# Kernel optimization log

Hardware: AMD Instinct MI355X
Metric: run time of the kernel (lower is better)

The kernel has to match this reference:

```python
import jax, jax.numpy as jnp
import numpy as np

N_IN = 20000
N_OUT = 20000
E = 640000
B = 64


def setup_inputs() -> dict:
    key = jax.random.key(0)
    ks = jax.random.split(key, 6)
    x = jax.random.normal(ks[0], (B, N_IN), dtype=jnp.float32)
    alpha = jax.random.normal(ks[1], (1, N_IN), dtype=jnp.float32) * 0.01  # xavier-ish scale
    sigma = jax.random.uniform(ks[2], (N_IN,), dtype=jnp.float32, minval=0.5, maxval=1.5)
    inp_positions = jax.random.normal(ks[3], (N_IN, 3), dtype=jnp.float32)
    out_positions = jax.random.normal(ks[4], (N_OUT, 3), dtype=jnp.float32)
    dst = jax.random.randint(ks[5], (E,), 0, N_OUT, dtype=jnp.int64)
    src = jax.random.randint(jax.random.fold_in(ks[5], 1), (E,), 0, N_IN, dtype=jnp.int64)
    edge_index = jnp.stack([dst, src], axis=0)  # [2, E]: row0 -> out node, row1 -> in node
    return {"x": x, "alpha": alpha, "sigma": sigma,
            "inp_positions": inp_positions, "out_positions": out_positions,
            "edge_index": edge_index}


def reference(x, alpha, sigma, inp_positions, out_positions, edge_index):
    dst = edge_index[0]  # [E] indexes out_positions
    src = edge_index[1]  # [E] indexes inp_positions
    # Gaussian RBF edge weights: exp(-||p_in - p_out||^2 / sigma_src^2)
    d = inp_positions[src] - out_positions[dst]          # [E, 3]
    w = jnp.exp(-jnp.sum(d * d, axis=-1) / (sigma[src] ** 2))  # [E]
    # spmm: y[b, i] = sum_{e: dst=i} w_e * (alpha * x)[b, src_e]
    msg = (alpha * x)[:, src] * w                         # [B, E]
    y = jax.ops.segment_sum(msg.T, dst, num_segments=out_positions.shape[0])  # [N_out, B]
    return y.T                                            # [B, N_out]
```

## Files before the change

kernel.cpp:

```cpp
#include <hip/hip_runtime.h>
#include <hip/hip_fp16.h>

#define N_IN   20000
#define N_OUT  20000
#define NEDGE  640000
#define B      64
#define NB     1250
#define CAPB   32
#define BTOT   768
#define CHUNK  8192
#define PBLK   79

__global__ __launch_bounds__(256)
void prep_partition_kernel(const int* __restrict__ edge,
                           unsigned int* __restrict__ gbuf,
                           int* __restrict__ cnt2d,
                           const float* __restrict__ x,
                           const float* __restrict__ alpha,
                           const float* __restrict__ ipos,
                           const float* __restrict__ opos,
                           const float* __restrict__ sigma,
                           __half* __restrict__ xt,
                           float4* __restrict__ psrc4,
                           float4* __restrict__ pdst4) {
    const int t = threadIdx.x;
    if (blockIdx.x < PBLK) {
        __shared__ int cnt[NB];
        const int blk = blockIdx.x;
        const int e_base = blk * CHUNK;
        const int ne = min(CHUNK, NEDGE - e_base);
        for (int b = t; b < NB; b += 256) cnt[b] = 0;
        __syncthreads();
        #pragma unroll
        for (int k = 0; k < CHUNK / 4 / 256; ++k) {
            const int i4 = (t + 256 * k) * 4;
            if (i4 < ne) {
                const int4 d4 = *reinterpret_cast<const int4*>(edge + e_base + i4);
                const int4 s4 = *reinterpret_cast<const int4*>(edge + NEDGE + e_base + i4);
                const int ds[4] = {d4.x, d4.y, d4.z, d4.w};
                const int sr[4] = {s4.x, s4.y, s4.z, s4.w};
                #pragma unroll
                for (int j = 0; j < 4; ++j) {
                    const int bk = ds[j] >> 4;
                    const int slot = atomicAdd(&cnt[bk], 1);
                    if (slot < CAPB)
                        gbuf[((size_t)bk * PBLK + blk) * CAPB + slot] =
                            ((unsigned int)ds[j] << 16) | (unsigned int)sr[j];
                }
            }
        }
        __syncthreads();
        for (int b = t; b < NB; b += 256)
            cnt2d[blk * NB + b] = cnt[b];
    } else {
        const int pb = blockIdx.x - PBLK;
        const int g = pb * 256 + t;
        if (g < N_IN)
            psrc4[g] = make_float4(ipos[3 * g], ipos[3 * g + 1], ipos[3 * g + 2], sigma[g]);
        if (g < N_OUT)
            pdst4[g] = make_float4(opos[3 * g], opos[3 * g + 1], opos[3 * g + 2], 0.0f);

        __shared__ float tile[64][65];
        const int i0 = pb * 64;
        const int tx = t & 63;
        const int ty = t >> 6;
        const int i  = i0 + tx;
        const float a = (i < N_IN) ? alpha[i] : 0.0f;
        #pragma unroll
        for (int k = 0; k < 16; ++k) {
            const int b = ty + (k << 2);
            tile[b][tx] = (i < N_IN) ? a * x[(size_t)b * N_IN + i] : 0.0f;
        }
        __syncthreads();
        #pragma unroll
        for (int k = 0; k < 16; ++k) {
            const int ii = ty + (k << 2);
            const int gi = i0 + ii;
            if (gi < N_IN) xt[(size_t)gi * B + tx] = __float2half(tile[tx][ii]);
        }
    }
}

__global__ __launch_bounds__(256, 4)
void bucket_gather_kernel(const int* __restrict__ cnt2d,
                          const unsigned int* __restrict__ gbuf,
                          const float4* __restrict__ psrc4,
                          const float4* __restrict__ pdst4,
                          const __half* __restrict__ xt,
                          float* __restrict__ y) {
    __shared__ unsigned int   ebuf[BTOT];
    __shared__ float          sw[BTOT];
    __shared__ unsigned short ss[BTOT];
    __shared__ int            rcnt[PBLK];
    __shared__ int            rbase[PBLK + 1];
    __shared__ int            bins[16], bcnt[16], base[17];
    __shared__ float4         pd[16];
    __shared__ float          tile[16][65];
    const int t = threadIdx.x;
    const int g = blockIdx.x;

    if (t < 16) { bins[t] = 0; bcnt[t] = 0; pd[t] = pdst4[g * 16 + t]; }
    if (t < PBLK) rcnt[t] = min(cnt2d[t * NB + g], CAPB);
    __syncthreads();
    if (t == 0) {
        int s = 0;
        for (int r = 0; r < PBLK; ++r) { rbase[r] = s; s += rcnt[r]; }
        rbase[PBLK] = s;
    }
    __syncthreads();
    const int ne = min(rbase[PBLK], BTOT);

    for (int idx = t; idx < PBLK * CAPB; idx += 256) {
        const int r = idx >> 5;
        const int s = idx & (CAPB - 1);
        if (s < rcnt[r]) {
            const int pos = rbase[r] + s;
            if (pos < BTOT) {
                const unsigned int u = gbuf[((size_t)g * PBLK + r) * CAPB + s];
                ebuf[pos] = u;
                atomicAdd(&bins[(u >> 16) & 15], 1);
            }
        }
    }
    __syncthreads();
    if (t == 0) {
        int s = 0;
        #pragma unroll
        for (int j = 0; j < 16; ++j) { base[j] = s; s += bins[j]; }
        base[16] = s;
    }
    __syncthreads();

    for (int i = t; i < ne; i += 256) {
        const unsigned int u = ebuf[i];
        const int src = u & 0xffffu;
        const int dl  = (u >> 16) & 15;
        const float4 ps = psrc4[src];
        const float dx = ps.x - pd[dl].x;
        const float dy = ps.y - pd[dl].y;
        const float dz = ps.z - pd[dl].z;
        const float w  = __expf(-(dx * dx + dy * dy + dz * dz) / (ps.w * ps.w));
        const int r = base[dl] + atomicAdd(&bcnt[dl], 1);
        sw[r] = w;
        ss[r] = (unsigned short)src;
    }
    __syncthreads();

    const int lane = t & 63;
    const int wv   = t >> 6;
    #pragma unroll
    for (int q = 0; q < 4; ++q) {
        const int dl = wv * 4 + q;
        int k = base[dl];
        const int end = base[dl + 1];
        float acc0 = 0.0f, acc1 = 0.0f;
        for (; k + 8 <= end; k += 8) {
            const int   s0 = ss[k],     s1 = ss[k + 1];
            const int   s2 = ss[k + 2], s3 = ss[k + 3];
            const int   s4 = ss[k + 4], s5 = ss[k + 5];
            const int   s6 = ss[k + 6], s7 = ss[k + 7];
            const float w0 = sw[k],     w1 = sw[k + 1];
            const float w2 = sw[k + 2], w3 = sw[k + 3];
            const float w4 = sw[k + 4], w5 = sw[k + 5];
            const float w6 = sw[k + 6], w7 = sw[k + 7];
            const float v0 = __half2float(xt[(size_t)s0 * B + lane]);
            const float v1 = __half2float(xt[(size_t)s1 * B + lane]);
            const float v2 = __half2float(xt[(size_t)s2 * B + lane]);
            const float v3 = __half2float(xt[(size_t)s3 * B + lane]);
            const float v4 = __half2float(xt[(size_t)s4 * B + lane]);
            const float v5 = __half2float(xt[(size_t)s5 * B + lane]);
            const float v6 = __half2float(xt[(size_t)s6 * B + lane]);
            const float v7 = __half2float(xt[(size_t)s7 * B + lane]);
            acc0 = fmaf(w0, v0, acc0);
            acc1 = fmaf(w1, v1, acc1);
            acc0 = fmaf(w2, v2, acc0);
            acc1 = fmaf(w3, v3, acc1);
            acc0 = fmaf(w4, v4, acc0);
            acc1 = fmaf(w5, v5, acc1);
            acc0 = fmaf(w6, v6, acc0);
            acc1 = fmaf(w7, v7, acc1);
        }
        for (; k < end; ++k)
            acc0 = fmaf(sw[k], __half2float(xt[(size_t)ss[k] * B + lane]), acc0);
        tile[dl][lane] = acc0 + acc1;
    }
    __syncthreads();

    const int j  = t & 15;
    const int b0 = t >> 4;
    #pragma unroll
    for (int p = 0; p < 4; ++p) {
        const int b = b0 * 4 + p;
        y[(size_t)b * N_OUT + g * 16 + j] = tile[j][b];
    }
}

extern "C" void kernel_launch(void* const* d_in, const int* in_sizes, int n_in,
                              void* d_out, int out_size, void* d_ws, size_t ws_size,
                              hipStream_t stream) {
    const float* x     = (const float*)d_in[0];
    const float* alpha = (const float*)d_in[1];
    const float* sigma = (const float*)d_in[2];
    const float* ipos  = (const float*)d_in[3];
    const float* opos  = (const float*)d_in[4];
    const int*   edge  = (const int*)d_in[5];
    float* y = (float*)d_out;

    __half*       xt    = (__half*)d_ws;
    unsigned int* gbuf  = (unsigned int*)(xt + (size_t)N_IN * B);
    float4*       psrc4 = (float4*)(gbuf + (size_t)NB * PBLK * CAPB);
    float4*       pdst4 = psrc4 + N_IN;
    int*          cnt2d = (int*)(pdst4 + N_OUT);

    prep_partition_kernel<<<PBLK + 313, 256, 0, stream>>>(
        edge, gbuf, cnt2d, x, alpha, ipos, opos, sigma, xt, psrc4, pdst4);
    bucket_gather_kernel<<<NB, 256, 0, stream>>>(
        cnt2d, gbuf, psrc4, pdst4, xt, y);
}
```

Measured before the change: 41.08 us.

## Halve partition chunk size, parallelize row-base scan, vectorize gather to half2 per lane

```diff
diff --git a/kernel.cpp b/kernel.cpp
--- a/kernel.cpp
+++ b/kernel.cpp
@@ -6,10 +6,10 @@
 #define NEDGE  640000
 #define B      64
 #define NB     1250
-#define CAPB   32
+#define CAPB   24
+#define CHUNK  4096
+#define PBLK   157
 #define BTOT   768
-#define CHUNK  8192
-#define PBLK   79
 
 __global__ __launch_bounds__(256)
 void prep_partition_kernel(const int* __restrict__ edge,
@@ -93,6 +93,7 @@
     __shared__ unsigned short ss[BTOT];
     __shared__ int            rcnt[PBLK];
     __shared__ int            rbase[PBLK + 1];
+    __shared__ int            sc[256];
     __shared__ int            bins[16], bcnt[16], base[17];
     __shared__ float4         pd[16];
     __shared__ float          tile[16][65];
@@ -102,17 +103,24 @@
     if (t < 16) { bins[t] = 0; bcnt[t] = 0; pd[t] = pdst4[g * 16 + t]; }
     if (t < PBLK) rcnt[t] = min(cnt2d[t * NB + g], CAPB);
     __syncthreads();
-    if (t == 0) {
-        int s = 0;
-        for (int r = 0; r < PBLK; ++r) { rbase[r] = s; s += rcnt[r]; }
-        rbase[PBLK] = s;
-    }
+
+    sc[t] = (t < PBLK) ? rcnt[t] : 0;
+    __syncthreads();
+    #pragma unroll
+    for (int d = 1; d < 256; d <<= 1) {
+        const int v = (t >= d) ? sc[t - d] : 0;
+        __syncthreads();
+        sc[t] += v;
+        __syncthreads();
+    }
+    if (t < PBLK) rbase[t] = sc[t] - rcnt[t];
+    if (t == 0) rbase[PBLK] = sc[PBLK - 1];
     __syncthreads();
     const int ne = min(rbase[PBLK], BTOT);
 
     for (int idx = t; idx < PBLK * CAPB; idx += 256) {
-        const int r = idx >> 5;
-        const int s = idx & (CAPB - 1);
+        const int r = idx / CAPB;
+        const int s = idx - r * CAPB;
         if (s < rcnt[r]) {
             const int pos = rbase[r] + s;
             if (pos < BTOT) {
@@ -148,6 +156,9 @@
 
     const int lane = t & 63;
     const int wv   = t >> 6;
+    const int half = lane >> 5;
+    const int l5   = lane & 31;
+    const unsigned int* xt2 = (const unsigned int*)xt;
     #pragma unroll
     for (int q = 0; q < 4; ++q) {
         const int dl = wv * 4 + q;
@@ -155,34 +166,38 @@
         const int end = base[dl + 1];
         float acc0 = 0.0f, acc1 = 0.0f;
         for (; k + 8 <= end; k += 8) {
-            const int   s0 = ss[k],     s1 = ss[k + 1];
-            const int   s2 = ss[k + 2], s3 = ss[k + 3];
-            const int   s4 = ss[k + 4], s5 = ss[k + 5];
-            const int   s6 = ss[k + 6], s7 = ss[k + 7];
-            const float w0 = sw[k],     w1 = sw[k + 1];
-            const float w2 = sw[k + 2], w3 = sw[k + 3];
-            const float w4 = sw[k + 4], w5 = sw[k + 5];
-            const float w6 = sw[k + 6], w7 = sw[k + 7];
-            const float v0 = __half2float(xt[(size_t)s0 * B + lane]);
-            const float v1 = __half2float(xt[(size_t)s1 * B + lane]);
-            const float v2 = __half2float(xt[(size_t)s2 * B + lane]);
-            const float v3 = __half2float(xt[(size_t)s3 * B + lane]);
-            const float v4 = __half2float(xt[(size_t)s4 * B + lane]);
-            const float v5 = __half2float(xt[(size_t)s5 * B + lane]);
-            const float v6 = __half2float(xt[(size_t)s6 * B + lane]);
-            const float v7 = __half2float(xt[(size_t)s7 * B + lane]);
-            acc0 = fmaf(w0, v0, acc0);
-            acc1 = fmaf(w1, v1, acc1);
-            acc0 = fmaf(w2, v2, acc0);
-            acc1 = fmaf(w3, v3, acc1);
-            acc0 = fmaf(w4, v4, acc0);
-            acc1 = fmaf(w5, v5, acc1);
-            acc0 = fmaf(w6, v6, acc0);
-            acc1 = fmaf(w7, v7, acc1);
-        }
-        for (; k < end; ++k)
-            acc0 = fmaf(sw[k], __half2float(xt[(size_t)ss[k] * B + lane]), acc0);
-        tile[dl][lane] = acc0 + acc1;
+            #pragma unroll
+            for (int j = 0; j < 4; ++j) {
+                const int ka = k + 2 * j;
+                const int   sA = ss[ka],     sB = ss[ka + 1];
+                const float wA = sw[ka],     wB = sw[ka + 1];
+                const int   sS = half ? sB : sA;
+                const float wS = half ? wB : wA;
+                const unsigned int p = xt2[(size_t)sS * 32 + l5];
+                const float2 f2 = __half22float2(*(const __half2*)&p);
+                acc0 = fmaf(wS, f2.x, acc0);
+                acc1 = fmaf(wS, f2.y, acc1);
+            }
+        }
+        for (; k < end; k += 2) {
+            const int   sA = ss[k];
+            const bool  hasB = (k + 1) < end;
+            const int   sB = hasB ? ss[k + 1] : sA;
+            const float wA = sw[k];
+            const float wB = hasB ? sw[k + 1] : 0.0f;
+            const int   sS = half ? sB : sA;
+            const float wS = half ? wB : wA;
+            const unsigned int p = xt2[(size_t)sS * 32 + l5];
+            const float2 f2 = __half22float2(*(const __half2*)&p);
+            acc0 = fmaf(wS, f2.x, acc0);
+            acc1 = fmaf(wS, f2.y, acc1);
+        }
+        acc0 += __shfl_xor(acc0, 32, 64);
+        acc1 += __shfl_xor(acc1, 32, 64);
+        if (half == 0) {
+            tile[dl][2 * l5]     = acc0;
+            tile[dl][2 * l5 + 1] = acc1;
+        }
     }
     __syncthreads();
 
```

Result: slower. 42.88 us (+4.4%).
